# Performance work log

Measured on AMD Instinct MI355X. Metric: run time of the kernel, lower is better.

Reference implementation:

```python
import jax, jax.numpy as jnp
import numpy as np

N = 100000   # nodes
E = 1600000  # edges
F = 128      # input node features
H = 128      # hidden_dim (conv2 out = H//2)
B = 50       # graphs in batch
C = 10       # fault classes


def _glorot(key, shape):
    fan_in, fan_out = shape
    lim = jnp.sqrt(6.0 / (fan_in + fan_out)).astype(jnp.float32)
    return jax.random.uniform(key, shape, jnp.float32, -lim, lim)


def setup_inputs() -> dict:
    key = jax.random.key(0)
    ks = jax.random.split(key, 8)
    x = jax.random.normal(ks[0], (N, F), jnp.float32)
    edge_index = jax.random.randint(ks[1], (2, E), 0, N, jnp.int32)
    batch = jnp.sort(jax.random.randint(ks[2], (N,), 0, B, jnp.int32))
    return {
        "x": x,
        "edge_index": edge_index,
        "batch": batch,
        "W1": _glorot(ks[3], (F, H)),
        "b1": jnp.zeros((H,), jnp.float32),
        "W2": _glorot(ks[4], (H, H // 2)),
        "b2": jnp.zeros((H // 2,), jnp.float32),
        "Wfc": _glorot(ks[5], (H // 2, C)),
        "bfc": jnp.zeros((C,), jnp.float32),
    }


def gcn_conv(h_in, W, b, src, dst, num_nodes):
    """PyG GCNConv with add_self_loops=True, edge_weight=None (all ones).
    out_i = sum_{j->i} (d_i^-1/2 d_j^-1/2) (W^T x_j) + d_i^-1 (W^T x_i) + b,
    where d includes the self-loop (+1). Self-loop handled analytically to
    avoid concatenating N extra edges."""
    h = h_in @ W                                                   # [N, out]
    ones_e = jnp.ones((src.shape[0],), h.dtype)
    deg = 1.0 + jax.ops.segment_sum(ones_e, dst, num_segments=num_nodes)
    dinv = jax.lax.rsqrt(deg)                                      # deg >= 1
    norm = dinv[src] * dinv[dst]                                   # [E]
    msgs = h[src] * norm[:, None]                                  # [E, out] gather
    agg = jax.ops.segment_sum(msgs, dst, num_segments=num_nodes)   # scatter-add
    return agg + h * (1.0 / deg)[:, None] + b


def reference(x, edge_index, batch, W1, b1, W2, b2, Wfc, bfc):
    src, dst = edge_index[0], edge_index[1]
    h = jax.nn.relu(gcn_conv(x, W1, b1, src, dst, N))
    # dropout(0.3) is identity in eval mode
    h = jax.nn.relu(gcn_conv(h, W2, b2, src, dst, N))
    # global mean pool over graphs
    sums = jax.ops.segment_sum(h, batch, num_segments=B)           # [B, H//2]
    counts = jax.ops.segment_sum(jnp.ones((N,), h.dtype), batch, num_segments=B)
    pooled = sums / jnp.maximum(counts, 1.0)[:, None]
    return pooled @ Wfc + bfc                                      # [B, C]
```

## Files before the change

kernel.cpp:

```cpp
#include <hip/hip_runtime.h>


#define IDX (blockIdx.x * (int)blockDim.x + (int)threadIdx.x)

__device__ __forceinline__ unsigned short f2bf(float f) {
    union { float f; unsigned u; } c{f};
    unsigned u = c.u;
    return (unsigned short)((u + 0x7fffu + ((u >> 16) & 1u)) >> 16);
}

__global__ void count_deg(const int* __restrict__ dst, int* __restrict__ cnt, int E) {
    int e = IDX;
    if (e < E) atomicAdd(&cnt[dst[e]], 1);
}

__global__ void compute_dinv(const int* __restrict__ cnt, float* __restrict__ dinv, int n) {
    int i = IDX;
    if (i < n) dinv[i] = 1.0f / sqrtf(1.0f + (float)cnt[i]);
}

__global__ void scan1(const int* __restrict__ cnt, int* __restrict__ rs,
                      int* __restrict__ bsum, int n) {
    __shared__ int lds[256];
    int t = threadIdx.x;
    int base = blockIdx.x * 1024 + t * 4;
    int c0 = 0, c1 = 0, c2 = 0, c3 = 0;
    if (base + 3 < n) {
        int4 v = *(const int4*)&cnt[base];
        c0 = v.x; c1 = v.y; c2 = v.z; c3 = v.w;
    } else {
        if (base     < n) c0 = cnt[base];
        if (base + 1 < n) c1 = cnt[base + 1];
        if (base + 2 < n) c2 = cnt[base + 2];
        if (base + 3 < n) c3 = cnt[base + 3];
    }
    int s = c0 + c1 + c2 + c3;
    lds[t] = s; __syncthreads();
    for (int off = 1; off < 256; off <<= 1) {
        int v = (t >= off) ? lds[t - off] : 0;
        __syncthreads();
        lds[t] += v;
        __syncthreads();
    }
    int incl = lds[t];
    int excl = incl - s;
    if (t == 255) bsum[blockIdx.x] = incl;
    if (base     < n) rs[base]     = excl;
    if (base + 1 < n) rs[base + 1] = excl + c0;
    if (base + 2 < n) rs[base + 2] = excl + c0 + c1;
    if (base + 3 < n) rs[base + 3] = excl + c0 + c1 + c2;
}

__global__ void scan2(int* __restrict__ bsum, int nb) {
    __shared__ int lds[128];
    int t = threadIdx.x;
    int v = (t < nb) ? bsum[t] : 0;
    lds[t] = v; __syncthreads();
    for (int off = 1; off < 128; off <<= 1) {
        int u = (t >= off) ? lds[t - off] : 0;
        __syncthreads();
        lds[t] += u;
        __syncthreads();
    }
    if (t < nb) bsum[t] = lds[t] - v;
}

__global__ void scan3(int* __restrict__ rs, const int* __restrict__ bsum, int n, int E) {
    int i = IDX;
    if (i < n) rs[i] += bsum[i >> 10];
    if (i == 0) rs[n] = E;
}

__global__ void fill_csr(const int* __restrict__ src, const int* __restrict__ dst,
                         const int* __restrict__ rs, int* __restrict__ cursor,
                         int* __restrict__ csr, int E) {
    int e = IDX;
    if (e < E) {
        int d = dst[e];
        int p = rs[d] + atomicAdd(&cursor[d], 1);
        csr[p] = src[e];
    }
}

__global__ __launch_bounds__(256) void gemm_k128_bf(const float* __restrict__ X,
        const float* __restrict__ W, const float* __restrict__ dinv,
        unsigned short* __restrict__ Ybf, int nrows, int outw) {
    __shared__ float ws[128][64];
    __shared__ float xs[64][128];
    const int t = threadIdx.x;
    const int row0 = blockIdx.x * 64;
    const int c0 = blockIdx.y * 64;

    #pragma unroll
    for (int i = 0; i < 8; ++i) {
        int idx = i * 256 + t;
        int k = idx >> 4, cq = idx & 15;
        float4 v = *(const float4*)&W[(size_t)k * outw + c0 + cq * 4];
        *(float4*)&ws[k][cq * 4] = v;
    }
    #pragma unroll
    for (int i = 0; i < 8; ++i) {
        int idx = i * 256 + t;
        int r = idx >> 5, kq = idx & 31;
        float4 v = make_float4(0.f, 0.f, 0.f, 0.f);
        if (row0 + r < nrows) v = *(const float4*)&X[(size_t)(row0 + r) * 128 + kq * 4];
        *(float4*)&xs[r][kq * 4] = v;
    }
    __syncthreads();

    const int r0  = (t >> 4) * 4;
    const int cc0 = (t & 15) * 4;
    float acc[4][4] = {};
    #pragma unroll 2
    for (int k0 = 0; k0 < 128; k0 += 4) {
        float xv[4][4], wv[4][4];
        #pragma unroll
        for (int i = 0; i < 4; ++i)
            *(float4*)xv[i] = *(const float4*)&xs[r0 + i][k0];
        #pragma unroll
        for (int kk = 0; kk < 4; ++kk)
            *(float4*)wv[kk] = *(const float4*)&ws[k0 + kk][cc0];
        #pragma unroll
        for (int i = 0; i < 4; ++i)
            #pragma unroll
            for (int kk = 0; kk < 4; ++kk)
                #pragma unroll
                for (int j = 0; j < 4; ++j)
                    acc[i][j] = fmaf(xv[i][kk], wv[kk][j], acc[i][j]);
    }
    #pragma unroll
    for (int i = 0; i < 4; ++i) {
        int row = row0 + r0 + i;
        if (row < nrows) {
            float s = dinv[row];
            ushort4 st;
            st.x = f2bf(acc[i][0] * s); st.y = f2bf(acc[i][1] * s);
            st.z = f2bf(acc[i][2] * s); st.w = f2bf(acc[i][3] * s);
            *(ushort4*)&Ybf[(size_t)row * outw + c0 + cc0] = st;
        }
    }
}

template<int FW, bool POOL>
__global__ __launch_bounds__(256) void aggregate_bf(
        const unsigned short* __restrict__ hbf, const int* __restrict__ rs,
        const int* __restrict__ csr, const float* __restrict__ dinv,
        const float* __restrict__ bias, const int* __restrict__ batch,
        float* __restrict__ pooled, float* __restrict__ out, int n) {
    int node = blockIdx.x * 4 + ((int)threadIdx.x >> 6);
    int lane = (int)threadIdx.x & 63;
    if (node >= n) return;
    const int b0 = rs[node], b1 = rs[node + 1];

    float a0 = 0.f, a1 = 0.f;
    int e = b0;
    for (; e + 8 <= b1; e += 8) {
        int s0 = csr[e],   s1 = csr[e+1], s2 = csr[e+2], s3 = csr[e+3];
        int s4 = csr[e+4], s5 = csr[e+5], s6 = csr[e+6], s7 = csr[e+7];
        if (FW == 128) {
            unsigned v0 = *(const unsigned*)&hbf[(size_t)s0*128 + lane*2];
            unsigned v1 = *(const unsigned*)&hbf[(size_t)s1*128 + lane*2];
            unsigned v2 = *(const unsigned*)&hbf[(size_t)s2*128 + lane*2];
            unsigned v3 = *(const unsigned*)&hbf[(size_t)s3*128 + lane*2];
            unsigned v4 = *(const unsigned*)&hbf[(size_t)s4*128 + lane*2];
            unsigned v5 = *(const unsigned*)&hbf[(size_t)s5*128 + lane*2];
            unsigned v6 = *(const unsigned*)&hbf[(size_t)s6*128 + lane*2];
            unsigned v7 = *(const unsigned*)&hbf[(size_t)s7*128 + lane*2];
            a0 += (__uint_as_float(v0 << 16) + __uint_as_float(v1 << 16))
                + (__uint_as_float(v2 << 16) + __uint_as_float(v3 << 16))
                + (__uint_as_float(v4 << 16) + __uint_as_float(v5 << 16))
                + (__uint_as_float(v6 << 16) + __uint_as_float(v7 << 16));
            a1 += (__uint_as_float(v0 & 0xffff0000u) + __uint_as_float(v1 & 0xffff0000u))
                + (__uint_as_float(v2 & 0xffff0000u) + __uint_as_float(v3 & 0xffff0000u))
                + (__uint_as_float(v4 & 0xffff0000u) + __uint_as_float(v5 & 0xffff0000u))
                + (__uint_as_float(v6 & 0xffff0000u) + __uint_as_float(v7 & 0xffff0000u));
        } else {
            unsigned u0 = hbf[(size_t)s0*64 + lane], u1 = hbf[(size_t)s1*64 + lane];
            unsigned u2 = hbf[(size_t)s2*64 + lane], u3 = hbf[(size_t)s3*64 + lane];
            unsigned u4 = hbf[(size_t)s4*64 + lane], u5 = hbf[(size_t)s5*64 + lane];
            unsigned u6 = hbf[(size_t)s6*64 + lane], u7 = hbf[(size_t)s7*64 + lane];
            a0 += (__uint_as_float(u0 << 16) + __uint_as_float(u1 << 16))
                + (__uint_as_float(u2 << 16) + __uint_as_float(u3 << 16))
                + (__uint_as_float(u4 << 16) + __uint_as_float(u5 << 16))
                + (__uint_as_float(u6 << 16) + __uint_as_float(u7 << 16));
        }
    }
    for (; e < b1; ++e) {
        int s = csr[e];
        if (FW == 128) {
            unsigned v = *(const unsigned*)&hbf[(size_t)s*128 + lane*2];
            a0 += __uint_as_float(v << 16);
            a1 += __uint_as_float(v & 0xffff0000u);
        } else {
            a0 += __uint_as_float((unsigned)hbf[(size_t)s*64 + lane] << 16);
        }
    }

    const float dn = dinv[node];
    if (FW == 128) {
        unsigned vs = *(const unsigned*)&hbf[(size_t)node*128 + lane*2];
        a0 += __uint_as_float(vs << 16);
        a1 += __uint_as_float(vs & 0xffff0000u);
        float2 bv = *(const float2*)&bias[lane*2];
        float o0 = fmaxf(fmaf(a0, dn, bv.x), 0.f);
        float o1 = fmaxf(fmaf(a1, dn, bv.y), 0.f);
        *(float2*)&out[(size_t)node*128 + lane*2] = make_float2(o0, o1);
    } else {
        a0 += __uint_as_float((unsigned)hbf[(size_t)node*64 + lane] << 16);
        float o = fmaxf(fmaf(a0, dn, bias[lane]), 0.f);
        if (POOL) atomicAdd(&pooled[(size_t)batch[node]*64 + lane], o);
        else out[(size_t)node*64 + lane] = o;
    }
}

__global__ void graph_counts(const int* __restrict__ batch, int* __restrict__ cntB,
                             int n, int B) {
    int b = (int)threadIdx.x;
    if (b < B) {
        int lo = 0, hi = n;
        while (lo < hi) { int mid = (lo + hi) >> 1; if (batch[mid] < b) lo = mid + 1; else hi = mid; }
        int start = lo;
        lo = 0; hi = n;
        while (lo < hi) { int mid = (lo + hi) >> 1; if (batch[mid] <= b) lo = mid + 1; else hi = mid; }
        cntB[b] = lo - start;
    }
}

__global__ void fc_kernel(const float* __restrict__ pooled, const int* __restrict__ cntB,
                          const float* __restrict__ Wfc, const float* __restrict__ bfc,
                          float* __restrict__ out) {
    int t = IDX;
    if (t < 50 * 10) {
        int b = t / 10, c = t % 10;
        float inv = 1.0f / fmaxf((float)cntB[b], 1.0f);
        float s = bfc[c];
        #pragma unroll
        for (int f = 0; f < 64; ++f)
            s = fmaf(pooled[b*64 + f] * inv, Wfc[f*10 + c], s);
        out[t] = s;
    }
}

extern "C" void kernel_launch(void* const* d_in, const int* in_sizes, int n_in,
                              void* d_out, int out_size, void* d_ws, size_t ws_size,
                              hipStream_t stream) {
    const float* x     = (const float*)d_in[0];
    const int*   ei    = (const int*)d_in[1];
    const int*   batch = (const int*)d_in[2];
    const float* W1    = (const float*)d_in[3];
    const float* b1    = (const float*)d_in[4];
    const float* W2    = (const float*)d_in[5];
    const float* b2    = (const float*)d_in[6];
    const float* Wfc   = (const float*)d_in[7];
    const float* bfc   = (const float*)d_in[8];
    float* out = (float*)d_out;

    const int n = in_sizes[2];
    const int E = in_sizes[1] / 2;
    const int* src = ei;
    const int* dst = ei + E;

    char* p = (char*)d_ws;
    auto alloc = [&](size_t bytes) { char* r = p; p += (bytes + 255) & ~(size_t)255; return r; };
    int*   cnt     = (int*)  alloc((size_t)n * 4);
    int*   cursor  = (int*)  alloc((size_t)n * 4);
    float* pooled  = (float*)alloc(50 * 64 * 4);
    size_t zbytes  = (size_t)(p - (char*)d_ws);
    int*   cntB    = (int*)  alloc(50 * 4);
    int*   bsum    = (int*)  alloc(128 * 4);
    int*   rs      = (int*)  alloc((size_t)(n + 1) * 4);
    int*   csr     = (int*)  alloc((size_t)E * 4);
    float* dinv    = (float*)alloc((size_t)n * 4);
    unsigned short* hbf1 = (unsigned short*)alloc((size_t)n * 128 * 2);
    unsigned short* hbf2 = (unsigned short*)alloc((size_t)n * 64 * 2);
    float* h_act   = (float*)alloc((size_t)n * 128 * 4);

    hipMemsetAsync(d_ws, 0, zbytes, stream);

    int eb    = (E + 255) / 256;
    int nb256 = (n + 255) / 256;
    int nscan = (n + 1023) / 1024;

    count_deg<<<eb, 256, 0, stream>>>(dst, cnt, E);
    compute_dinv<<<nb256, 256, 0, stream>>>(cnt, dinv, n);
    scan1<<<nscan, 256, 0, stream>>>(cnt, rs, bsum, n);
    scan2<<<1, 128, 0, stream>>>(bsum, nscan);
    scan3<<<nb256, 256, 0, stream>>>(rs, bsum, n, E);
    fill_csr<<<eb, 256, 0, stream>>>(src, dst, rs, cursor, csr, E);

    dim3 g1((n + 63) / 64, 2);
    gemm_k128_bf<<<g1, 256, 0, stream>>>(x, W1, dinv, hbf1, n, 128);
    int nagg = (n + 3) / 4;
    aggregate_bf<128, false><<<nagg, 256, 0, stream>>>(hbf1, rs, csr, dinv,
                                                       b1, batch, pooled, h_act, n);

    dim3 g2((n + 63) / 64, 1);
    gemm_k128_bf<<<g2, 256, 0, stream>>>(h_act, W2, dinv, hbf2, n, 64);
    graph_counts<<<1, 64, 0, stream>>>(batch, cntB, n, 50);
    aggregate_bf<64, true><<<nagg, 256, 0, stream>>>(hbf2, rs, csr, dinv,
                                                     b2, batch, pooled, nullptr, n);

    fc_kernel<<<1, 512, 0, stream>>>(pooled, cntB, Wfc, bfc, out);
}
```

Before: 650.1 us.

## Pad CSR rows to multiples of eight with sentinel zero row

Rounds each node's neighbour count up to a multiple of eight in the row-offset scan and fills the padding slots with a sentinel index that points at an extra all-zero feature row. The aggregation loop then runs without a scalar tail and loads neighbour indices as aligned int4 vectors. In exchange it adds a CSR initialisation pass over a larger array, and the padded slots trigger extra gathers of the zero row, which add memory traffic on top of the real edges.

```diff
diff --git a/kernel.cpp b/kernel.cpp
--- a/kernel.cpp
+++ b/kernel.cpp
@@ -20,20 +20,15 @@
 }
 
 __global__ void scan1(const int* __restrict__ cnt, int* __restrict__ rs,
-                      int* __restrict__ bsum, int n) {
+                      int* __restrict__ bsum, int n, int m) {
     __shared__ int lds[256];
     int t = threadIdx.x;
     int base = blockIdx.x * 1024 + t * 4;
     int c0 = 0, c1 = 0, c2 = 0, c3 = 0;
-    if (base + 3 < n) {
-        int4 v = *(const int4*)&cnt[base];
-        c0 = v.x; c1 = v.y; c2 = v.z; c3 = v.w;
-    } else {
-        if (base     < n) c0 = cnt[base];
-        if (base + 1 < n) c1 = cnt[base + 1];
-        if (base + 2 < n) c2 = cnt[base + 2];
-        if (base + 3 < n) c3 = cnt[base + 3];
-    }
+    if (base     < n) c0 = (cnt[base]     + 7) & ~7;
+    if (base + 1 < n) c1 = (cnt[base + 1] + 7) & ~7;
+    if (base + 2 < n) c2 = (cnt[base + 2] + 7) & ~7;
+    if (base + 3 < n) c3 = (cnt[base + 3] + 7) & ~7;
     int s = c0 + c1 + c2 + c3;
     lds[t] = s; __syncthreads();
     for (int off = 1; off < 256; off <<= 1) {
@@ -45,10 +40,10 @@
     int incl = lds[t];
     int excl = incl - s;
     if (t == 255) bsum[blockIdx.x] = incl;
-    if (base     < n) rs[base]     = excl;
-    if (base + 1 < n) rs[base + 1] = excl + c0;
-    if (base + 2 < n) rs[base + 2] = excl + c0 + c1;
-    if (base + 3 < n) rs[base + 3] = excl + c0 + c1 + c2;
+    if (base     < m) rs[base]     = excl;
+    if (base + 1 < m) rs[base + 1] = excl + c0;
+    if (base + 2 < m) rs[base + 2] = excl + c0 + c1;
+    if (base + 3 < m) rs[base + 3] = excl + c0 + c1 + c2;
 }
 
 __global__ void scan2(int* __restrict__ bsum, int nb) {
@@ -65,10 +60,14 @@
     if (t < nb) bsum[t] = lds[t] - v;
 }
 
-__global__ void scan3(int* __restrict__ rs, const int* __restrict__ bsum, int n, int E) {
+__global__ void scan3(int* __restrict__ rs, const int* __restrict__ bsum, int m) {
     int i = IDX;
-    if (i < n) rs[i] += bsum[i >> 10];
-    if (i == 0) rs[n] = E;
+    if (i < m) rs[i] += bsum[i >> 10];
+}
+
+__global__ void csr_init(int* __restrict__ csr, int sentinel, int len) {
+    int i = IDX;
+    if (i < len) csr[i] = sentinel;
 }
 
 __global__ void fill_csr(const int* __restrict__ src, const int* __restrict__ dst,
@@ -80,6 +79,13 @@
         int p = rs[d] + atomicAdd(&cursor[d], 1);
         csr[p] = src[e];
     }
+}
+
+__global__ void zero_pad_rows(unsigned short* __restrict__ hbf1,
+                              unsigned short* __restrict__ hbf2, int n) {
+    int t = (int)threadIdx.x;
+    if (t < 128) hbf1[(size_t)n * 128 + t] = 0;
+    if (t < 64)  hbf2[(size_t)n * 64 + t] = 0;
 }
 
 __global__ __launch_bounds__(256) void gemm_k128_bf(const float* __restrict__ X,
@@ -153,19 +159,18 @@
     const int b0 = rs[node], b1 = rs[node + 1];
 
     float a0 = 0.f, a1 = 0.f;
-    int e = b0;
-    for (; e + 8 <= b1; e += 8) {
-        int s0 = csr[e],   s1 = csr[e+1], s2 = csr[e+2], s3 = csr[e+3];
-        int s4 = csr[e+4], s5 = csr[e+5], s6 = csr[e+6], s7 = csr[e+7];
+    for (int e = b0; e < b1; e += 8) {
+        int4 ia = *(const int4*)&csr[e];
+        int4 ib = *(const int4*)&csr[e + 4];
         if (FW == 128) {
-            unsigned v0 = *(const unsigned*)&hbf[(size_t)s0*128 + lane*2];
-            unsigned v1 = *(const unsigned*)&hbf[(size_t)s1*128 + lane*2];
-            unsigned v2 = *(const unsigned*)&hbf[(size_t)s2*128 + lane*2];
-            unsigned v3 = *(const unsigned*)&hbf[(size_t)s3*128 + lane*2];
-            unsigned v4 = *(const unsigned*)&hbf[(size_t)s4*128 + lane*2];
-            unsigned v5 = *(const unsigned*)&hbf[(size_t)s5*128 + lane*2];
-            unsigned v6 = *(const unsigned*)&hbf[(size_t)s6*128 + lane*2];
-            unsigned v7 = *(const unsigned*)&hbf[(size_t)s7*128 + lane*2];
+            unsigned v0 = *(const unsigned*)&hbf[(size_t)ia.x*128 + lane*2];
+            unsigned v1 = *(const unsigned*)&hbf[(size_t)ia.y*128 + lane*2];
+            unsigned v2 = *(const unsigned*)&hbf[(size_t)ia.z*128 + lane*2];
+            unsigned v3 = *(const unsigned*)&hbf[(size_t)ia.w*128 + lane*2];
+            unsigned v4 = *(const unsigned*)&hbf[(size_t)ib.x*128 + lane*2];
+            unsigned v5 = *(const unsigned*)&hbf[(size_t)ib.y*128 + lane*2];
+            unsigned v6 = *(const unsigned*)&hbf[(size_t)ib.z*128 + lane*2];
+            unsigned v7 = *(const unsigned*)&hbf[(size_t)ib.w*128 + lane*2];
             a0 += (__uint_as_float(v0 << 16) + __uint_as_float(v1 << 16))
                 + (__uint_as_float(v2 << 16) + __uint_as_float(v3 << 16))
                 + (__uint_as_float(v4 << 16) + __uint_as_float(v5 << 16))
@@ -175,24 +180,14 @@
                 + (__uint_as_float(v4 & 0xffff0000u) + __uint_as_float(v5 & 0xffff0000u))
                 + (__uint_as_float(v6 & 0xffff0000u) + __uint_as_float(v7 & 0xffff0000u));
         } else {
-            unsigned u0 = hbf[(size_t)s0*64 + lane], u1 = hbf[(size_t)s1*64 + lane];
-            unsigned u2 = hbf[(size_t)s2*64 + lane], u3 = hbf[(size_t)s3*64 + lane];
-            unsigned u4 = hbf[(size_t)s4*64 + lane], u5 = hbf[(size_t)s5*64 + lane];
-            unsigned u6 = hbf[(size_t)s6*64 + lane], u7 = hbf[(size_t)s7*64 + lane];
+            unsigned u0 = hbf[(size_t)ia.x*64 + lane], u1 = hbf[(size_t)ia.y*64 + lane];
+            unsigned u2 = hbf[(size_t)ia.z*64 + lane], u3 = hbf[(size_t)ia.w*64 + lane];
+            unsigned u4 = hbf[(size_t)ib.x*64 + lane], u5 = hbf[(size_t)ib.y*64 + lane];
+            unsigned u6 = hbf[(size_t)ib.z*64 + lane], u7 = hbf[(size_t)ib.w*64 + lane];
             a0 += (__uint_as_float(u0 << 16) + __uint_as_float(u1 << 16))
                 + (__uint_as_float(u2 << 16) + __uint_as_float(u3 << 16))
                 + (__uint_as_float(u4 << 16) + __uint_as_float(u5 << 16))
                 + (__uint_as_float(u6 << 16) + __uint_as_float(u7 << 16));
-        }
-    }
-    for (; e < b1; ++e) {
-        int s = csr[e];
-        if (FW == 128) {
-            unsigned v = *(const unsigned*)&hbf[(size_t)s*128 + lane*2];
-            a0 += __uint_as_float(v << 16);
-            a1 += __uint_as_float(v & 0xffff0000u);
-        } else {
-            a0 += __uint_as_float((unsigned)hbf[(size_t)s*64 + lane] << 16);
         }
     }
 
@@ -257,6 +252,7 @@
 
     const int n = in_sizes[2];
     const int E = in_sizes[1] / 2;
+    const int Epad = E + 8 * n;
     const int* src = ei;
     const int* dst = ei + E;
 
@@ -269,24 +265,29 @@
     int*   cntB    = (int*)  alloc(50 * 4);
     int*   bsum    = (int*)  alloc(128 * 4);
     int*   rs      = (int*)  alloc((size_t)(n + 1) * 4);
-    int*   csr     = (int*)  alloc((size_t)E * 4);
+    int*   csr     = (int*)  alloc((size_t)Epad * 4);
     float* dinv    = (float*)alloc((size_t)n * 4);
-    unsigned short* hbf1 = (unsigned short*)alloc((size_t)n * 128 * 2);
-    unsigned short* hbf2 = (unsigned short*)alloc((size_t)n * 64 * 2);
+    unsigned short* hbf1 = (unsigned short*)alloc((size_t)(n + 1) * 128 * 2);
+    unsigned short* hbf2 = (unsigned short*)alloc((size_t)(n + 1) * 64 * 2);
     float* h_act   = (float*)alloc((size_t)n * 128 * 4);
 
     hipMemsetAsync(d_ws, 0, zbytes, stream);
 
+    const int m = n + 1;
     int eb    = (E + 255) / 256;
+    int epb   = (Epad + 255) / 256;
     int nb256 = (n + 255) / 256;
-    int nscan = (n + 1023) / 1024;
+    int mb256 = (m + 255) / 256;
+    int nscan = (m + 1023) / 1024;
 
     count_deg<<<eb, 256, 0, stream>>>(dst, cnt, E);
     compute_dinv<<<nb256, 256, 0, stream>>>(cnt, dinv, n);
-    scan1<<<nscan, 256, 0, stream>>>(cnt, rs, bsum, n);
+    scan1<<<nscan, 256, 0, stream>>>(cnt, rs, bsum, n, m);
     scan2<<<1, 128, 0, stream>>>(bsum, nscan);
-    scan3<<<nb256, 256, 0, stream>>>(rs, bsum, n, E);
+    scan3<<<mb256, 256, 0, stream>>>(rs, bsum, m);
+    csr_init<<<epb, 256, 0, stream>>>(csr, n, Epad);
     fill_csr<<<eb, 256, 0, stream>>>(src, dst, rs, cursor, csr, E);
+    zero_pad_rows<<<1, 128, 0, stream>>>(hbf1, hbf2, n);
 
     dim3 g1((n + 63) / 64, 2);
     gemm_k128_bf<<<g1, 256, 0, stream>>>(x, W1, dinv, hbf1, n, 128);
```

New measurement: 645.6 us. Within noise of the previous version (-0.7%).
